# Performance work log

Measured on AMD Instinct MI355X. Metric: run time of the kernel, lower is better.

The kernel has to match this reference:

```python
import jax, jax.numpy as jnp
import numpy as np

B, T, D, H = 2, 2048, 2048, 16
d_head = D // H  # 128


def _rope(x):
    # x: [B, T, H, d]
    d = x.shape[-1]
    inv_freq = 1.0 / (10000.0 ** (jnp.arange(0, d, 2, dtype=jnp.float32) / d))
    t = jnp.arange(x.shape[1], dtype=jnp.float32)
    freqs = t[:, None] * inv_freq[None, :]          # [T, d/2]
    emb = jnp.concatenate([freqs, freqs], axis=-1)  # [T, d]
    cos = jnp.cos(emb)[None, :, None, :]
    sin = jnp.sin(emb)[None, :, None, :]
    x1, x2 = x[..., ::2], x[..., 1::2]
    rot = jnp.stack([-x2, x1], axis=-1).reshape(x.shape)
    return x * cos + rot * sin


def setup_inputs() -> dict:
    key = jax.random.key(0)
    ks = jax.random.split(key, 8)
    s = 1.0 / np.sqrt(D)
    return {
        "x": jax.random.normal(ks[0], (B, T, D), dtype=jnp.float32),
        "W_q": jax.random.normal(ks[1], (D, D), dtype=jnp.float32) * s,
        "W_k": jax.random.normal(ks[2], (D, D), dtype=jnp.float32) * s,
        "W_v": jax.random.normal(ks[3], (D, D), dtype=jnp.float32) * s,
        "W_gate": jax.random.normal(ks[4], (D, D), dtype=jnp.float32) * s,
        "W_p": jax.random.normal(ks[5], (D, D), dtype=jnp.float32) * s,
        "W_clock": jax.random.normal(ks[6], (D, H), dtype=jnp.float32) * s,
        "W_c": jax.random.normal(ks[7], (D, D), dtype=jnp.float32) * s,
    }


def _caps_forward(x, W_q, W_k, W_v, W_gate, W_p, W_clock, W_c):
    Bx, Tx, Dx = x.shape
    q = (x @ W_q).reshape(Bx, Tx, H, d_head)
    k = (x @ W_k).reshape(Bx, Tx, H, d_head)
    v = (x @ W_v).reshape(Bx, Tx, H, d_head)

    clock = jax.nn.softplus(x @ W_clock).reshape(Bx, Tx, H, 1) + 1e-6
    log_clock = jnp.log(clock)

    q = _rope(q)
    k = _rope(k)

    # Branch 1: p_exp normalization
    p = (x @ W_p).reshape(Bx, Tx, H, d_head) + log_clock
    p_max = jnp.max(p, axis=1, keepdims=True)
    p_exp = jnp.exp(p - p_max)
    p_cs = jnp.cumsum(p_exp, axis=1)
    q1 = q / (p_cs + 1e-8)
    k1 = k * p_exp

    # Branch 2: SPD gate cumprod via clipped cumsum
    gj = -jax.nn.softplus(x @ W_gate).reshape(Bx, Tx, H, d_head) * clock
    gj_cp = jnp.exp(jnp.clip(jnp.cumsum(gj, axis=1), -50.0, 40.0))
    q2 = q * gj_cp
    k2 = k / (gj_cp + 1e-8)

    # Branch 3: clock time scaling
    clock_cs = jnp.cumsum(clock, axis=1)
    q3 = q / clock_cs
    k3 = k * clock

    q_cat = jnp.concatenate([q1, q2, q3], axis=-1)  # [B,T,H,3d]
    k_cat = jnp.concatenate([k1, k2, k3], axis=-1)

    scale = 1.0 / jnp.sqrt(jnp.float32(3 * d_head))  # SDPA default: 1/sqrt(q last dim)
    scores = jnp.einsum('bthd,bshd->bhts', q_cat, k_cat) * scale
    attn = jax.nn.softmax(scores, axis=-1)
    out = jnp.einsum('bhts,bshd->bthd', attn, v).reshape(Bx, Tx, Dx)
    return out @ W_c


def reference(x, W_q, W_k, W_v, W_gate, W_p, W_clock, W_c):
    return _caps_forward(x, W_q, W_k, W_v, W_gate, W_p, W_clock, W_c)
```

## Files before the change

kernel.cpp:

```cpp
#include <hip/hip_runtime.h>

typedef unsigned short ushort;
typedef __attribute__((ext_vector_type(8))) short short8;
typedef __attribute__((ext_vector_type(4))) short short4v;
typedef __attribute__((ext_vector_type(4))) float f32x4;

#define Bb 2
#define Tt 2048
#define Dd 2048
#define Hh 16
#define Mm 4096
#define MD 8388608u

__device__ __forceinline__ float b2f(ushort u) {
  union { unsigned int ui; float f; } v; v.ui = ((unsigned int)u) << 16; return v.f;
}
__device__ __forceinline__ ushort f2b(float f) {
  union { float f; unsigned int u; } v; v.f = f;
  unsigned int r = (v.u + 0x7fffu + ((v.u >> 16) & 1u)) >> 16;
  return (ushort)r;
}
__device__ __forceinline__ void split3(float v, ushort& s0, ushort& s1, ushort& s2) {
  ushort a = f2b(v);        float f0 = b2f(a);
  float r1 = v - f0;        ushort b = f2b(r1);  float f1 = b2f(b);
  float r2 = r1 - f1;       ushort c = f2b(r2);
  s0 = a; s1 = b; s2 = c;
}
__device__ __forceinline__ void split3_rtz(float v, ushort& s0, ushort& s1, ushort& s2) {
  union { float f; unsigned u; } c; c.f = v;
  s0 = (ushort)(c.u >> 16);
  union { unsigned u; float f; } h; h.u = c.u & 0xffff0000u;
  float r1 = v - h.f;
  union { float f; unsigned u; } c1; c1.f = r1;
  s1 = (ushort)(c1.u >> 16);
  union { unsigned u; float f; } h1; h1.u = c1.u & 0xffff0000u;
  float r2 = r1 - h1.f;
  s2 = f2b(r2);
}
__device__ __forceinline__ void split2(float v, ushort& s0, ushort& s1) {
  union { float f; unsigned u; } c; c.f = v;
  s0 = (ushort)(c.u >> 16);
  union { unsigned u; float f; } h; h.u = c.u & 0xffff0000u;
  s1 = f2b(v - h.f);
}
__device__ __forceinline__ float softplusf(float x) {
  return fmaxf(x, 0.f) + log1pf(expf(-fabsf(x)));
}
__device__ __forceinline__ short4v tr16(unsigned a) {
  short4v d;
  asm volatile("ds_read_b64_tr_b16 %0, %1" : "=v"(d) : "v"(a));
  return d;
}

__global__ __launch_bounds__(256) void xsplit_k(const float* __restrict__ x,
                                                ushort* __restrict__ S0,
                                                ushort* __restrict__ S1,
                                                ushort* __restrict__ S2) {
  size_t i = ((size_t)blockIdx.x * 256 + threadIdx.x) * 8;
  float v[8];
  *(float4*)&v[0] = *(const float4*)(x + i);
  *(float4*)&v[4] = *(const float4*)(x + i + 4);
  ushort h0[8], h1[8], h2[8];
#pragma unroll
  for (int j = 0; j < 8; ++j) split3_rtz(v[j], h0[j], h1[j], h2[j]);
  *(uint4*)(S0 + i) = *(uint4*)h0;
  *(uint4*)(S1 + i) = *(uint4*)h1;
  *(uint4*)(S2 + i) = *(uint4*)h2;
}

template <int NP>
__global__ __launch_bounds__(256) void split_transposeN(const float* __restrict__ W,
                                                        ushort* __restrict__ T0,
                                                        ushort* __restrict__ T1,
                                                        ushort* __restrict__ T2) {
  __shared__ float tile[64][68];
  int k0 = blockIdx.x << 6, n0 = blockIdx.y << 6;
  int r = threadIdx.x >> 2, c0 = (threadIdx.x & 3) << 4;
  const float* src = W + (size_t)(k0 + r) * Dd + n0 + c0;
#pragma unroll
  for (int q = 0; q < 4; ++q)
    *(float4*)&tile[r][c0 + 4 * q] = *(const float4*)(src + 4 * q);
  __syncthreads();
  ushort h0[16], h1[16], h2[16];
#pragma unroll
  for (int i = 0; i < 16; ++i) {
    float v = tile[c0 + i][r];
    if (NP == 1) {
      h0[i] = f2b(v);
    } else if (NP == 2) {
      ushort a = f2b(v); h0[i] = a; h1[i] = f2b(v - b2f(a));
    } else {
      split3(v, h0[i], h1[i], h2[i]);
    }
  }
  size_t o = (size_t)(n0 + r) * Dd + k0 + c0;
  *(uint4*)(T0 + o) = *(uint4*)&h0[0];  *(uint4*)(T0 + o + 8) = *(uint4*)&h0[8];
  if (NP >= 2) { *(uint4*)(T1 + o) = *(uint4*)&h1[0];  *(uint4*)(T1 + o + 8) = *(uint4*)&h1[8]; }
  if (NP >= 3) { *(uint4*)(T2 + o) = *(uint4*)&h2[0];  *(uint4*)(T2 + o + 8) = *(uint4*)&h2[8]; }
}

__global__ __launch_bounds__(512) void gemm128_pre2(const ushort* __restrict__ A0,
                                                    const ushort* __restrict__ A1,
                                                    const ushort* __restrict__ B0,
                                                    const ushort* __restrict__ B1,
                                                    float* __restrict__ C) {
  const int N = 2048, K = 2048;
  int m0 = blockIdx.y << 7, n0 = blockIdx.x << 7;
  __shared__ ushort As0[8192], As1[8192], Bs0[8192], Bs1[8192];
  int tid = threadIdx.x;
  int row = tid >> 2, c0 = (tid & 3) << 4;
  int sw = row & 7, g0 = c0 >> 3;
  int dst0 = row * 64 + ((g0 ^ sw) << 3);
  int dst1 = row * 64 + (((g0 + 1) ^ sw) << 3);
  const ushort* a0p = A0 + (size_t)(m0 + row) * K + c0;
  const ushort* a1p = A1 + (size_t)(m0 + row) * K + c0;
  const ushort* b0p = B0 + (size_t)(n0 + row) * K + c0;
  const ushort* b1p = B1 + (size_t)(n0 + row) * K + c0;
  int lane = tid & 63, wave = tid >> 6;
  int l16 = lane & 15, quad = lane >> 4;
  int wm = (wave & 1) << 6, wn = (wave >> 1) << 5;
  f32x4 acc[4][2] = {};
  for (int k0 = 0; k0 < K; k0 += 64) {
    uint4 a00 = *(const uint4*)(a0p + k0), a01 = *(const uint4*)(a0p + k0 + 8);
    uint4 a10 = *(const uint4*)(a1p + k0), a11 = *(const uint4*)(a1p + k0 + 8);
    uint4 b00 = *(const uint4*)(b0p + k0), b01 = *(const uint4*)(b0p + k0 + 8);
    uint4 b10 = *(const uint4*)(b1p + k0), b11 = *(const uint4*)(b1p + k0 + 8);
    *(uint4*)&As0[dst0] = a00;  *(uint4*)&As0[dst1] = a01;
    *(uint4*)&As1[dst0] = a10;  *(uint4*)&As1[dst1] = a11;
    *(uint4*)&Bs0[dst0] = b00;  *(uint4*)&Bs0[dst1] = b01;
    *(uint4*)&Bs1[dst0] = b10;  *(uint4*)&Bs1[dst1] = b11;
    __syncthreads();
#pragma unroll
    for (int kk = 0; kk < 2; ++kk) {
      short8 af0[4], af1[4], bf0[2], bf1[2];
#pragma unroll
      for (int mi = 0; mi < 4; ++mi) {
        int rr = wm + (mi << 4) + l16;
        int g = (kk << 2) + quad;
        int idx = rr * 64 + ((g ^ (rr & 7)) << 3);
        af0[mi] = *(const short8*)&As0[idx];
        af1[mi] = *(const short8*)&As1[idx];
      }
#pragma unroll
      for (int nj = 0; nj < 2; ++nj) {
        int rr = wn + (nj << 4) + l16;
        int g = (kk << 2) + quad;
        int idx = rr * 64 + ((g ^ (rr & 7)) << 3);
        bf0[nj] = *(const short8*)&Bs0[idx];
        bf1[nj] = *(const short8*)&Bs1[idx];
      }
#pragma unroll
      for (int mi = 0; mi < 4; ++mi)
#pragma unroll
        for (int nj = 0; nj < 2; ++nj) {
          acc[mi][nj] = __builtin_amdgcn_mfma_f32_16x16x32_bf16(af1[mi], bf0[nj], acc[mi][nj], 0, 0, 0);
          acc[mi][nj] = __builtin_amdgcn_mfma_f32_16x16x32_bf16(af0[mi], bf1[nj], acc[mi][nj], 0, 0, 0);
          acc[mi][nj] = __builtin_amdgcn_mfma_f32_16x16x32_bf16(af0[mi], bf0[nj], acc[mi][nj], 0, 0, 0);
        }
    }
    __syncthreads();
  }
#pragma unroll
  for (int mi = 0; mi < 4; ++mi)
#pragma unroll
    for (int nj = 0; nj < 2; ++nj)
#pragma unroll
      for (int r = 0; r < 4; ++r) {
        int mm = m0 + wm + (mi << 4) + (quad << 2) + r;
        int nn = n0 + wn + (nj << 4) + l16;
        C[(size_t)mm * N + nn] = acc[mi][nj][r];
      }
}

template <int BF16OUT>
__global__ __launch_bounds__(512) void gemm128_split2(const float* __restrict__ A,
                                                      const ushort* __restrict__ B0,
                                                      const ushort* __restrict__ B1,
                                                      void* __restrict__ CBase) {
  const int N = 2048, K = 2048;
  int m0 = blockIdx.y << 7, n0 = blockIdx.x << 7;
  __shared__ ushort As0[8192], As1[8192], Bs0[8192], Bs1[8192];
  int tid = threadIdx.x;
  int row = tid >> 2, c0 = (tid & 3) << 4;
  int sw = row & 7, g0 = c0 >> 3;
  int dst0 = row * 64 + ((g0 ^ sw) << 3);
  int dst1 = row * 64 + (((g0 + 1) ^ sw) << 3);
  const float* aptr = A + (size_t)(m0 + row) * K + c0;
  const ushort* b0p = B0 + (size_t)(n0 + row) * K + c0;
  const ushort* b1p = B1 + (size_t)(n0 + row) * K + c0;
  int lane = tid & 63, wave = tid >> 6;
  int l16 = lane & 15, quad = lane >> 4;
  int wm = (wave & 1) << 6, wn = (wave >> 1) << 5;
  f32x4 acc[4][2] = {};
  for (int k0 = 0; k0 < K; k0 += 64) {
    float av[16];
#pragma unroll
    for (int q = 0; q < 4; ++q)
      *(float4*)&av[4 * q] = *(const float4*)(aptr + k0 + 4 * q);
    ushort a0[16], a1[16];
#pragma unroll
    for (int i = 0; i < 16; ++i) split2(av[i], a0[i], a1[i]);
    uint4 b00 = *(const uint4*)(b0p + k0), b01 = *(const uint4*)(b0p + k0 + 8);
    uint4 b10 = *(const uint4*)(b1p + k0), b11 = *(const uint4*)(b1p + k0 + 8);
    *(uint4*)&As0[dst0] = *(uint4*)&a0[0];  *(uint4*)&As0[dst1] = *(uint4*)&a0[8];
    *(uint4*)&As1[dst0] = *(uint4*)&a1[0];  *(uint4*)&As1[dst1] = *(uint4*)&a1[8];
    *(uint4*)&Bs0[dst0] = b00;  *(uint4*)&Bs0[dst1] = b01;
    *(uint4*)&Bs1[dst0] = b10;  *(uint4*)&Bs1[dst1] = b11;
    __syncthreads();
#pragma unroll
    for (int kk = 0; kk < 2; ++kk) {
      short8 af0[4], af1[4], bf0[2], bf1[2];
#pragma unroll
      for (int mi = 0; mi < 4; ++mi) {
        int rr = wm + (mi << 4) + l16;
        int g = (kk << 2) + quad;
        int idx = rr * 64 + ((g ^ (rr & 7)) << 3);
        af0[mi] = *(const short8*)&As0[idx];
        af1[mi] = *(const short8*)&As1[idx];
      }
#pragma unroll
      for (int nj = 0; nj < 2; ++nj) {
        int rr = wn + (nj << 4) + l16;
        int g = (kk << 2) + quad;
        int idx = rr * 64 + ((g ^ (rr & 7)) << 3);
        bf0[nj] = *(const short8*)&Bs0[idx];
        bf1[nj] = *(const short8*)&Bs1[idx];
      }
#pragma unroll
      for (int mi = 0; mi < 4; ++mi)
#pragma unroll
        for (int nj = 0; nj < 2; ++nj) {
          acc[mi][nj] = __builtin_amdgcn_mfma_f32_16x16x32_bf16(af1[mi], bf0[nj], acc[mi][nj], 0, 0, 0);
          acc[mi][nj] = __builtin_amdgcn_mfma_f32_16x16x32_bf16(af0[mi], bf1[nj], acc[mi][nj], 0, 0, 0);
          acc[mi][nj] = __builtin_amdgcn_mfma_f32_16x16x32_bf16(af0[mi], bf0[nj], acc[mi][nj], 0, 0, 0);
        }
    }
    __syncthreads();
  }
#pragma unroll
  for (int mi = 0; mi < 4; ++mi)
#pragma unroll
    for (int nj = 0; nj < 2; ++nj)
#pragma unroll
      for (int r = 0; r < 4; ++r) {
        int mm = m0 + wm + (mi << 4) + (quad << 2) + r;
        int nn = n0 + wn + (nj << 4) + l16;
        float v = acc[mi][nj][r];
        if (BF16OUT)
          ((ushort*)CBase)[(size_t)mm * N + nn] = f2b(v);
        else
          ((float*)CBase)[(size_t)mm * N + nn] = v;
      }
}

__global__ __launch_bounds__(512) void gemm128_b16(const ushort* __restrict__ A,
                                                   const ushort* __restrict__ Bt,
                                                   float* __restrict__ C) {
  const int N = 2048, K = 2048;
  int m0 = blockIdx.y << 7, n0 = blockIdx.x << 7;
  __shared__ ushort As[8192], Bs[8192];
  int tid = threadIdx.x;
  int row = tid >> 2, c0 = (tid & 3) << 4;
  int sw = row & 7, g0 = c0 >> 3;
  int dst0 = row * 64 + ((g0 ^ sw) << 3);
  int dst1 = row * 64 + (((g0 + 1) ^ sw) << 3);
  const ushort* aptr = A + (size_t)(m0 + row) * K + c0;
  const ushort* bptr = Bt + (size_t)(n0 + row) * K + c0;
  int lane = tid & 63, wave = tid >> 6;
  int l16 = lane & 15, quad = lane >> 4;
  int wm = (wave & 1) << 6, wn = (wave >> 1) << 5;
  f32x4 acc[4][2] = {};
  for (int k0 = 0; k0 < K; k0 += 64) {
    uint4 av0 = *(const uint4*)(aptr + k0), av1 = *(const uint4*)(aptr + k0 + 8);
    uint4 bv0 = *(const uint4*)(bptr + k0), bv1 = *(const uint4*)(bptr + k0 + 8);
    *(uint4*)&As[dst0] = av0;  *(uint4*)&As[dst1] = av1;
    *(uint4*)&Bs[dst0] = bv0;  *(uint4*)&Bs[dst1] = bv1;
    __syncthreads();
#pragma unroll
    for (int kk = 0; kk < 2; ++kk) {
      short8 af[4], bf[2];
#pragma unroll
      for (int mi = 0; mi < 4; ++mi) {
        int rr = wm + (mi << 4) + l16;
        int g = (kk << 2) + quad;
        af[mi] = *(const short8*)&As[rr * 64 + ((g ^ (rr & 7)) << 3)];
      }
#pragma unroll
      for (int nj = 0; nj < 2; ++nj) {
        int rr = wn + (nj << 4) + l16;
        int g = (kk << 2) + quad;
        bf[nj] = *(const short8*)&Bs[rr * 64 + ((g ^ (rr & 7)) << 3)];
      }
#pragma unroll
      for (int mi = 0; mi < 4; ++mi)
#pragma unroll
        for (int nj = 0; nj < 2; ++nj)
          acc[mi][nj] = __builtin_amdgcn_mfma_f32_16x16x32_bf16(af[mi], bf[nj], acc[mi][nj], 0, 0, 0);
    }
    __syncthreads();
  }
#pragma unroll
  for (int mi = 0; mi < 4; ++mi)
#pragma unroll
    for (int nj = 0; nj < 2; ++nj)
#pragma unroll
      for (int r = 0; r < 4; ++r) {
        int mm = m0 + wm + (mi << 4) + (quad << 2) + r;
        int nn = n0 + wn + (nj << 4) + l16;
        C[(size_t)mm * N + nn] = acc[mi][nj][r];
      }
}

__global__ __launch_bounds__(256) void gemm_pre(const ushort* __restrict__ A0,
                                                const ushort* __restrict__ A1,
                                                const ushort* __restrict__ A2,
                                                const ushort* __restrict__ B0,
                                                const ushort* __restrict__ B1,
                                                const ushort* __restrict__ B2,
                                                float* __restrict__ C) {
  const int N = 2048, K = 2048;
  int m0 = blockIdx.y << 6, n0 = blockIdx.x << 6;
  __shared__ ushort As0[4096], As1[4096], As2[4096];
  __shared__ ushort Bs0[4096], Bs1[4096], Bs2[4096];
  int tid = threadIdx.x;
  int row = tid >> 2, c0 = (tid & 3) << 4;
  int sw = row & 7;
  int g0 = c0 >> 3;
  int dst0 = row * 64 + ((g0 ^ sw) << 3);
  int dst1 = row * 64 + (((g0 + 1) ^ sw) << 3);
  const ushort* a0p = A0 + (size_t)(m0 + row) * K + c0;
  const ushort* a1p = A1 + (size_t)(m0 + row) * K + c0;
  const ushort* a2p = A2 + (size_t)(m0 + row) * K + c0;
  const ushort* b0p = B0 + (size_t)(n0 + row) * K + c0;
  const ushort* b1p = B1 + (size_t)(n0 + row) * K + c0;
  const ushort* b2p = B2 + (size_t)(n0 + row) * K + c0;
  int lane = tid & 63, wave = tid >> 6;
  int l16 = lane & 15, quad = lane >> 4;
  int wm = (wave & 1) << 5, wn = (wave >> 1) << 5;
  f32x4 acc[2][2] = {};
  for (int k0 = 0; k0 < K; k0 += 64) {
    uint4 a00 = *(const uint4*)(a0p + k0), a01 = *(const uint4*)(a0p + k0 + 8);
    uint4 a10 = *(const uint4*)(a1p + k0), a11 = *(const uint4*)(a1p + k0 + 8);
    uint4 a20 = *(const uint4*)(a2p + k0), a21 = *(const uint4*)(a2p + k0 + 8);
    uint4 b00 = *(const uint4*)(b0p + k0), b01 = *(const uint4*)(b0p + k0 + 8);
    uint4 b10 = *(const uint4*)(b1p + k0), b11 = *(const uint4*)(b1p + k0 + 8);
    uint4 b20 = *(const uint4*)(b2p + k0), b21 = *(const uint4*)(b2p + k0 + 8);
    *(uint4*)&As0[dst0] = a00;  *(uint4*)&As0[dst1] = a01;
    *(uint4*)&As1[dst0] = a10;  *(uint4*)&As1[dst1] = a11;
    *(uint4*)&As2[dst0] = a20;  *(uint4*)&As2[dst1] = a21;
    *(uint4*)&Bs0[dst0] = b00;  *(uint4*)&Bs0[dst1] = b01;
    *(uint4*)&Bs1[dst0] = b10;  *(uint4*)&Bs1[dst1] = b11;
    *(uint4*)&Bs2[dst0] = b20;  *(uint4*)&Bs2[dst1] = b21;
    __syncthreads();
#pragma unroll
    for (int kk = 0; kk < 2; ++kk) {
      short8 af0[2], af1[2], af2[2], bf0[2], bf1[2], bf2[2];
#pragma unroll
      for (int mi = 0; mi < 2; ++mi) {
        int rr = wm + (mi << 4) + l16;
        int g = (kk << 2) + quad;
        int idx = rr * 64 + ((g ^ (rr & 7)) << 3);
        af0[mi] = *(const short8*)&As0[idx];
        af1[mi] = *(const short8*)&As1[idx];
        af2[mi] = *(const short8*)&As2[idx];
      }
#pragma unroll
      for (int nj = 0; nj < 2; ++nj) {
        int rr = wn + (nj << 4) + l16;
        int g = (kk << 2) + quad;
        int idx = rr * 64 + ((g ^ (rr & 7)) << 3);
        bf0[nj] = *(const short8*)&Bs0[idx];
        bf1[nj] = *(const short8*)&Bs1[idx];
        bf2[nj] = *(const short8*)&Bs2[idx];
      }
#pragma unroll
      for (int mi = 0; mi < 2; ++mi)
#pragma unroll
        for (int nj = 0; nj < 2; ++nj) {
          acc[mi][nj] = __builtin_amdgcn_mfma_f32_16x16x32_bf16(af2[mi], bf0[nj], acc[mi][nj], 0, 0, 0);
          acc[mi][nj] = __builtin_amdgcn_mfma_f32_16x16x32_bf16(af0[mi], bf2[nj], acc[mi][nj], 0, 0, 0);
          acc[mi][nj] = __builtin_amdgcn_mfma_f32_16x16x32_bf16(af1[mi], bf1[nj], acc[mi][nj], 0, 0, 0);
          acc[mi][nj] = __builtin_amdgcn_mfma_f32_16x16x32_bf16(af1[mi], bf0[nj], acc[mi][nj], 0, 0, 0);
          acc[mi][nj] = __builtin_amdgcn_mfma_f32_16x16x32_bf16(af0[mi], bf1[nj], acc[mi][nj], 0, 0, 0);
          acc[mi][nj] = __builtin_amdgcn_mfma_f32_16x16x32_bf16(af0[mi], bf0[nj], acc[mi][nj], 0, 0, 0);
        }
    }
    __syncthreads();
  }
#pragma unroll
  for (int mi = 0; mi < 2; ++mi)
#pragma unroll
    for (int nj = 0; nj < 2; ++nj)
#pragma unroll
      for (int r = 0; r < 4; ++r) {
        int mm = m0 + wm + (mi << 4) + (quad << 2) + r;
        int nn = n0 + wn + (nj << 4) + l16;
        C[(size_t)mm * N + nn] = acc[mi][nj][r];
      }
}

__global__ __launch_bounds__(64) void wclock_k(const float* __restrict__ x,
                                               const float* __restrict__ Wc,
                                               float* __restrict__ out) {
  int m = blockIdx.x, lane = threadIdx.x;
  const float* xr = x + (size_t)m * Dd;
  float acc[16];
#pragma unroll
  for (int h = 0; h < 16; ++h) acc[h] = 0.f;
  for (int k = lane; k < Dd; k += 64) {
    float xv = xr[k];
    const float* wr = Wc + k * 16;
#pragma unroll
    for (int h = 0; h < 16; ++h) acc[h] += xv * wr[h];
  }
#pragma unroll
  for (int h = 0; h < 16; ++h) {
#pragma unroll
    for (int off = 32; off; off >>= 1) acc[h] += __shfl_down(acc[h], off);
  }
  if (lane == 0) {
    float* o = out + (size_t)m * 16;
#pragma unroll
    for (int h = 0; h < 16; ++h) o[h] = acc[h];
  }
}

__global__ __launch_bounds__(128) void pmaxchunk_k(const float* __restrict__ Pf,
                                                   const float* __restrict__ cpre,
                                                   float* __restrict__ pmaxc) {
  int bh = blockIdx.x, ch = blockIdx.y, d = threadIdx.x;
  int b = bh >> 4, h = bh & 15;
  float mx = -1e30f;
  int t0 = ch << 8;
  for (int t = t0; t < t0 + 256; ++t) {
    float pr = Pf[((size_t)(b * Tt + t)) * Dd + h * 128 + d];
    float c = softplusf(cpre[(b * Tt + t) * Hh + h]) + 1e-6f;
    mx = fmaxf(mx, pr + logf(c));
  }
  pmaxc[(size_t)(bh * 8 + ch) * 128 + d] = mx;
}

__global__ __launch_bounds__(128) void scan_ew_k(float* planes,
                                                 const float* __restrict__ cpre,
                                                 const float* __restrict__ pmaxc,
                                                 float* __restrict__ clockv,
                                                 float* __restrict__ sum_pe,
                                                 float* __restrict__ sum_gj,
                                                 float* __restrict__ sum_ck) {
  int ch = blockIdx.x, bh = blockIdx.y;
  int b = bh >> 4, h = bh & 15, d = threadIdx.x;
  float* Qf = planes;
  float* Kf = planes + (size_t)MD;
  float* Gf = planes + 2 * (size_t)MD;
  float* Pf = planes + 3 * (size_t)MD;
  float invf = (float)exp(-((double)((d & 63) * 2) / 128.0) * log(10000.0));
  float pmax = -1e30f;
#pragma unroll
  for (int c = 0; c < 8; ++c) pmax = fmaxf(pmax, pmaxc[(size_t)(bh * 8 + c) * 128 + d]);
  float s_pe = 0.f, s_gj = 0.f, s_ck = 0.f;
  int t0 = ch << 5;
#pragma unroll 4
  for (int i = 0; i < 32; ++i) {
    int t = t0 + i;
    size_t off = ((size_t)(b * Tt + t)) * Dd + h * 128 + d;
    float qv = Qf[off], kv = Kf[off], pv = Pf[off], gv = Gf[off];
    float clock = softplusf(cpre[(b * Tt + t) * Hh + h]) + 1e-6f;
    float ang = (float)t * invf;
    float c_ = cosf(ang), s_ = sinf(ang);
    float qp = __shfl_xor(qv, 1);
    float kp = __shfl_xor(kv, 1);
    float qrot = (d & 1) ? qp : -qp;
    float krot = (d & 1) ? kp : -kp;
    float qr = qv * c_ + qrot * s_;
    float kr = kv * c_ + krot * s_;
    float pe = expf(pv + logf(clock) - pmax);
    s_pe += pe;
    float gj = -softplusf(gv) * clock;
    s_gj += gj;
    Qf[off] = qr;
    Kf[off] = kr;
    Gf[off] = gj;
    Pf[off] = pe;
    if (d == 0) {
      clockv[bh * Tt + t] = clock;
      s_ck += clock;
    }
  }
  size_t so = (size_t)(bh * 64 + ch) * 128 + d;
  sum_pe[so] = s_pe;
  sum_gj[so] = s_gj;
  if (d == 0) sum_ck[bh * 64 + ch] = s_ck;
}

__global__ __launch_bounds__(128) void scan_off_k(const float* __restrict__ sum_pe,
                                                  const float* __restrict__ sum_gj,
                                                  const float* __restrict__ sum_ck,
                                                  float* __restrict__ pcs_cp,
                                                  float* __restrict__ goff,
                                                  float* __restrict__ coff) {
  int bh = blockIdx.x, d = threadIdx.x;
  float ppe = 0.f, pgj = 0.f, pck = 0.f;
  for (int c = 0; c < 64; ++c) {
    size_t o = (size_t)(bh * 64 + c) * 128 + d;
    pcs_cp[o] = ppe;
    goff[o] = pgj;
    ppe += sum_pe[o];
    pgj += sum_gj[o];
    if (d == 0) { coff[bh * 64 + c] = pck; pck += sum_ck[bh * 64 + c]; }
  }
}

__global__ __launch_bounds__(128) void scan_apply_k(float* planes,
                                                    const float* __restrict__ goff,
                                                    const float* __restrict__ coff,
                                                    const float* __restrict__ clockv,
                                                    float* __restrict__ ccsv) {
  int ch = blockIdx.x, bh = blockIdx.y;
  int b = bh >> 4, h = bh & 15, d = threadIdx.x;
  float* Gf = planes + 2 * (size_t)MD;
  float g = goff[(size_t)(bh * 64 + ch) * 128 + d];
  float ccs = (d == 0) ? coff[bh * 64 + ch] : 0.f;
  int t0 = ch << 5;
#pragma unroll 4
  for (int i = 0; i < 32; ++i) {
    int t = t0 + i;
    size_t off = ((size_t)(b * Tt + t)) * Dd + h * 128 + d;
    float gj = Gf[off];
    g += gj;
    float e = expf(fminf(fmaxf(g, -50.f), 40.f));
    Gf[off] = e;
    if (d == 0) {
      ccs += clockv[bh * Tt + t];
      ccsv[bh * Tt + t] = ccs;
    }
  }
}

__global__ __launch_bounds__(512, 2) void attn_mfma_k(const float* __restrict__ planes,
                                                      const ushort* __restrict__ Vb,
                                                      const float* __restrict__ clockv,
                                                      const float* __restrict__ ccsv,
                                                      const float* __restrict__ pcs_cp,
                                                      ushort* __restrict__ attnout) {
  __shared__ float smemf[18432];
  ushort* Khi = (ushort*)smemf;
  ushort* Klo = Khi + 12288;
  ushort* Vsm = Khi + 24576;
  unsigned* Pu = (unsigned*)(smemf + 14336);
  float* pcsL = smemf;
  ushort* qscr = (ushort*)(smemf + 8192);

  int tid = threadIdx.x;
  int lane = tid & 63, wave = tid >> 6;
  int l15 = lane & 15, qd = lane >> 4;
  int qt0 = blockIdx.x << 7;
  int bh = blockIdx.y, b = bh >> 4, h = bh & 15;
  const float* Qf = planes;
  const float* Kf = planes + (size_t)MD;
  const float* Ef = planes + 2 * (size_t)MD;
  const float* Pe = planes + 3 * (size_t)MD;
  size_t pbase = ((size_t)b * Tt) * Dd + h * 128;

  short8 qh[12], ql[12];
  int wl = wave & 3;
  int rloc = lane >> 2;
  {
    ushort* sh = qscr + (wl << 12);
    ushort* sl = sh + 2048;
#pragma unroll
    for (int rd = 0; rd < 2; ++rd) {
      if (tid < 256) {
        int d = tid & 127, seg = tid >> 7;
        int rbase = (rd << 6) + (seg << 5);
        float pcs = pcs_cp[((size_t)bh * 64 + (qt0 >> 5) + (rd << 1) + seg) * 128 + d];
        for (int i = 0; i < 32; ++i) {
          pcs += Pe[pbase + (size_t)(qt0 + rbase + i) * Dd + d];
          pcsL[((seg << 5) + i) * 128 + d] = pcs;
        }
      }
      __syncthreads();
      int part = ((wave >> 2) == rd);
      int grow = qt0 + (rd << 6) + (wl << 4) + rloc;
      float ccsr = __builtin_amdgcn_rcpf(ccsv[bh * Tt + grow]);
      size_t goffq = pbase + (size_t)grow * Dd;
#pragma unroll
      for (int cd = 0; cd < 3; ++cd) {
        __syncthreads();
        if (part) {
#pragma unroll
          for (int j = 0; j < 4; ++j) {
            int d0 = ((lane & 3) << 5) + (j << 3);
            float qv[8], mv[8];
            *(float4*)&qv[0] = *(const float4*)(Qf + goffq + d0);
            *(float4*)&qv[4] = *(const float4*)(Qf + goffq + d0 + 4);
            if (cd == 0) {
              *(float4*)&mv[0] = *(const float4*)&pcsL[((wl << 4) + rloc) * 128 + d0];
              *(float4*)&mv[4] = *(const float4*)&pcsL[((wl << 4) + rloc) * 128 + d0 + 4];
#pragma unroll
              for (int i = 0; i < 8; ++i) qv[i] = qv[i] * __builtin_amdgcn_rcpf(mv[i] + 1e-8f);
            } else if (cd == 1) {
              *(float4*)&mv[0] = *(const float4*)(Ef + goffq + d0);
              *(float4*)&mv[4] = *(const float4*)(Ef + goffq + d0 + 4);
#pragma unroll
              for (int i = 0; i < 8; ++i) qv[i] = qv[i] * mv[i];
            } else {
#pragma unroll
              for (int i = 0; i < 8; ++i) qv[i] = qv[i] * ccsr;
            }
            ushort hi8[8], lo8[8];
#pragma unroll
            for (int i = 0; i < 8; ++i) {
              ushort a = f2b(qv[i]); hi8[i] = a; lo8[i] = f2b(qv[i] - b2f(a));
            }
            int g = ((lane & 3) << 2) + j;
            int phys = (g & 8) | ((g ^ rloc) & 7);
            *(uint4*)&sh[rloc * 128 + (phys << 3)] = *(uint4*)hi8;
            *(uint4*)&sl[rloc * 128 + (phys << 3)] = *(uint4*)lo8;
          }
        }
        __syncthreads();
        if (part) {
#pragma unroll
          for (int ksl = 0; ksl < 4; ++ksl) {
            int g = (ksl << 2) + qd;
            int phys = (g & 8) | ((g ^ l15) & 7);
            qh[(cd << 2) + ksl] = *(const short8*)&sh[l15 * 128 + (phys << 3)];
            ql[(cd << 2) + ksl] = *(const short8*)&sl[l15 * 128 + (phys << 3)];
          }
        }
      }
      __syncthreads();
    }
  }

  float mi4[4], li4[4];
  f32x4 acc_pv[8] = {};
#pragma unroll
  for (int r = 0; r < 4; ++r) { mi4[r] = -1e30f; li4[r] = 0.f; }
  const float scl = 0.05103103630798287f;
  const ushort* vbase = Vb + pbase;
  unsigned* PuW = Pu + (wave << 9);
  unsigned VsmA = (unsigned)(size_t)Vsm;
  int kk = tid >> 4;
  int kdb = tid & 15;

  for (int st = 0; st < 64; ++st) {
    int s0 = st << 5;
    __syncthreads();
    {
      size_t roff = pbase + (size_t)(s0 + kk) * Dd + (kdb << 3);
      float ck = clockv[bh * Tt + s0 + kk];
      float kv[8], pev[8], ev[8];
      *(float4*)&kv[0] = *(const float4*)(Kf + roff);
      *(float4*)&kv[4] = *(const float4*)(Kf + roff + 4);
      *(float4*)&pev[0] = *(const float4*)(Pe + roff);
      *(float4*)&pev[4] = *(const float4*)(Pe + roff + 4);
      *(float4*)&ev[0] = *(const float4*)(Ef + roff);
      *(float4*)&ev[4] = *(const float4*)(Ef + roff + 4);
#pragma unroll
      for (int slot = 0; slot < 3; ++slot) {
        float val[8];
        if (slot == 0) {
#pragma unroll
          for (int i = 0; i < 8; ++i) val[i] = kv[i] * pev[i];
        } else if (slot == 1) {
#pragma unroll
          for (int i = 0; i < 8; ++i) val[i] = kv[i] * __builtin_amdgcn_rcpf(ev[i] + 1e-8f);
        } else {
#pragma unroll
          for (int i = 0; i < 8; ++i) val[i] = kv[i] * ck;
        }
        unsigned ub[8], ul[8];
#pragma unroll
        for (int i = 0; i < 8; ++i) {
          union { float f; unsigned u; } c; c.f = val[i];
          ub[i] = c.u;
          union { unsigned u; float f; } hm; hm.u = c.u & 0xffff0000u;
          union { float f; unsigned u; } lr; lr.f = val[i] - hm.f;
          ul[i] = lr.u;
        }
        uint4 hi4, lo4;
        hi4.x = (ub[0] >> 16) | (ub[1] & 0xffff0000u);
        hi4.y = (ub[2] >> 16) | (ub[3] & 0xffff0000u);
        hi4.z = (ub[4] >> 16) | (ub[5] & 0xffff0000u);
        hi4.w = (ub[6] >> 16) | (ub[7] & 0xffff0000u);
        lo4.x = (ul[0] >> 16) | (ul[1] & 0xffff0000u);
        lo4.y = (ul[2] >> 16) | (ul[3] & 0xffff0000u);
        lo4.z = (ul[4] >> 16) | (ul[5] & 0xffff0000u);
        lo4.w = (ul[6] >> 16) | (ul[7] & 0xffff0000u);
        int g = (slot << 4) + kdb;
        int phys = (g & ~7) | ((g ^ kk) & 7);
        *(uint4*)&Khi[kk * 384 + (phys << 3)] = hi4;
        *(uint4*)&Klo[kk * 384 + (phys << 3)] = lo4;
      }
      const ushort* vsrc = vbase + (size_t)(s0 + kk) * Dd + (kdb << 3);
      int vbyte = ((kdb >> 1) << 10) + (((kk >> 2) & 1) << 9) + ((kk >> 3) << 7) +
                  ((kk & 3) << 5) + ((kdb & 1) << 4);
      *(uint4*)((char*)Vsm + vbyte) = *(const uint4*)vsrc;
    }
    __syncthreads();
    f32x4 acc0 = {}, acc1 = {};
#pragma unroll
    for (int ks = 0; ks < 12; ++ks) {
      int g = (ks << 2) + qd;
      int p0i = (g & ~7) | ((g ^ l15) & 7);
      int p1i = (g & ~7) | ((g ^ (16 + l15)) & 7);
      short8 b0h = *(const short8*)&Khi[l15 * 384 + (p0i << 3)];
      short8 b0l = *(const short8*)&Klo[l15 * 384 + (p0i << 3)];
      short8 b1h = *(const short8*)&Khi[(16 + l15) * 384 + (p1i << 3)];
      short8 b1l = *(const short8*)&Klo[(16 + l15) * 384 + (p1i << 3)];
      acc0 = __builtin_amdgcn_mfma_f32_16x16x32_bf16(ql[ks], b0h, acc0, 0, 0, 0);
      acc0 = __builtin_amdgcn_mfma_f32_16x16x32_bf16(qh[ks], b0l, acc0, 0, 0, 0);
      acc0 = __builtin_amdgcn_mfma_f32_16x16x32_bf16(qh[ks], b0h, acc0, 0, 0, 0);
      acc1 = __builtin_amdgcn_mfma_f32_16x16x32_bf16(ql[ks], b1h, acc1, 0, 0, 0);
      acc1 = __builtin_amdgcn_mfma_f32_16x16x32_bf16(qh[ks], b1l, acc1, 0, 0, 0);
      acc1 = __builtin_amdgcn_mfma_f32_16x16x32_bf16(qh[ks], b1h, acc1, 0, 0, 0);
    }
#pragma unroll
    for (int r = 0; r < 4; ++r) {
      float sa = acc0[r] * scl, sb = acc1[r] * scl;
      float mx = fmaxf(sa, sb);
#pragma unroll
      for (int m = 1; m < 16; m <<= 1) mx = fmaxf(mx, __shfl_xor(mx, m));
      float mn = fmaxf(mi4[r], mx);
      float al = expf(mi4[r] - mn);
      float p0 = expf(sa - mn), p1 = expf(sb - mn);
      float rs = p0 + p1;
#pragma unroll
      for (int m = 1; m < 16; m <<= 1) rs += __shfl_xor(rs, m);
      li4[r] = li4[r] * al + rs;
      mi4[r] = mn;
#pragma unroll
      for (int n0 = 0; n0 < 8; ++n0) acc_pv[n0][r] *= al;
      int R = (qd << 2) + r;
      {
        union { float f; unsigned u; } c0, c1; c0.f = p0; c1.f = p1;
        union { unsigned u; float f; } m0_, m1_;
        m0_.u = c0.u & 0xffff0000u; m1_.u = c1.u & 0xffff0000u;
        union { float f; unsigned u; } d0_, d1_;
        d0_.f = p0 - m0_.f; d1_.f = p1 - m1_.f;
        unsigned u0 = (c0.u >> 16) | (d0_.u & 0xffff0000u);
        unsigned u1 = (c1.u >> 16) | (d1_.u & 0xffff0000u);
        int r7 = R & 7;
        char* pb = (char*)PuW + (R << 7) + ((l15 & 3) << 2);
        *(unsigned*)(pb + (((l15 >> 2) ^ r7) << 4)) = u0;
        *(unsigned*)(pb + ((((l15 >> 2) + 4) ^ r7) << 4)) = u1;
      }
    }
    {
      unsigned pw[8];
      {
        const char* pb = (const char*)PuW + l15 * 128;
        uint4 w0 = *(const uint4*)(pb + ((((qd << 1)) ^ (l15 & 7)) << 4));
        uint4 w1 = *(const uint4*)(pb + ((((qd << 1) | 1) ^ (l15 & 7)) << 4));
        pw[0] = w0.x; pw[1] = w0.y; pw[2] = w0.z; pw[3] = w0.w;
        pw[4] = w1.x; pw[5] = w1.y; pw[6] = w1.z; pw[7] = w1.w;
      }
      union { unsigned u[4]; short8 s; } uph, upl;
#pragma unroll
      for (int i = 0; i < 4; ++i) {
        uph.u[i] = (pw[2 * i] & 0xffffu) | (pw[2 * i + 1] << 16);
        upl.u[i] = (pw[2 * i] >> 16) | (pw[2 * i + 1] & 0xffff0000u);
      }
      short4v tv[16];
#pragma unroll
      for (int n0 = 0; n0 < 8; ++n0) {
        unsigned a0 = VsmA + (n0 << 10) + (lane << 3);
        tv[2 * n0] = tr16(a0);
        tv[2 * n0 + 1] = tr16(a0 + 512);
      }
      asm volatile("s_waitcnt lgkmcnt(0)" ::: "memory");
      __builtin_amdgcn_sched_barrier(0);
#pragma unroll
      for (int n0 = 0; n0 < 8; ++n0) {
        short8 bv = __builtin_shufflevector(tv[2 * n0], tv[2 * n0 + 1], 0, 1, 2, 3, 4, 5, 6, 7);
        acc_pv[n0] = __builtin_amdgcn_mfma_f32_16x16x32_bf16(uph.s, bv, acc_pv[n0], 0, 0, 0);
        acc_pv[n0] = __builtin_amdgcn_mfma_f32_16x16x32_bf16(upl.s, bv, acc_pv[n0], 0, 0, 0);
      }
    }
  }
#pragma unroll
  for (int r = 0; r < 4; ++r) {
    float inv = 1.f / li4[r];
    int trow = qt0 + (wave << 4) + (qd << 2) + r;
    ushort* orow = attnout + ((size_t)(b * Tt + trow)) * Dd + h * 128 + l15;
#pragma unroll
    for (int n0 = 0; n0 < 8; ++n0)
      orow[n0 << 4] = f2b(acc_pv[n0][r] * inv);
  }
}

extern "C" void kernel_launch(void* const* d_in, const int* in_sizes, int n_in,
                              void* d_out, int out_size, void* d_ws, size_t ws_size,
                              hipStream_t stream) {
  const float* x = (const float*)d_in[0];
  const float* Wq = (const float*)d_in[1];
  const float* Wk = (const float*)d_in[2];
  const float* Wv = (const float*)d_in[3];
  const float* Wg = (const float*)d_in[4];
  const float* Wp = (const float*)d_in[5];
  const float* Wclk = (const float*)d_in[6];
  const float* Wc = (const float*)d_in[7];

  float* planes = (float*)d_ws;
  float* Aq = planes;
  float* Bk = planes + (size_t)MD;
  float* Ce = planes + 2 * (size_t)MD;
  float* Dp = planes + 3 * (size_t)MD;
  ushort* Vb = (ushort*)(planes + 4 * (size_t)MD);
  float* cpre = (float*)(Vb + (size_t)MD);
  float* clockv = cpre + 65536;
  float* ccsv = clockv + 65536;
  float* pmaxc = ccsv + 65536;
  float* pcs_cp = pmaxc + 32768;
  ushort* Wt0 = (ushort*)(pcs_cp + 262144);
  ushort* Wt1 = Wt0 + (size_t)Dd * Dd;
  ushort* Wt2 = Wt1 + (size_t)Dd * Dd;
  ushort* attnout = Wt0;
  ushort* WcT0 = (ushort*)Ce;
  ushort* xs0 = (ushort*)Dp;
  ushort* xs1 = xs0 + (size_t)MD;
  ushort* xs2 = (ushort*)Vb;
  float* sum_pe = (float*)Wt2;
  float* sum_gj = sum_pe + 262144;
  float* goff_  = sum_gj + 262144;
  float* sum_ck = goff_ + 262144;
  float* coff_  = sum_ck + 2048;

  size_t needed = (size_t)((char*)(Wt2 + (size_t)Dd * Dd) - (char*)d_ws);
  if (ws_size < needed) return;

  dim3 tg(Dd / 64, Dd / 64);
  dim3 g128(Dd / 128, Mm / 128), gg(Dd / 64, Mm / 64);

  xsplit_k<<<dim3(MD / 8 / 256), 256, 0, stream>>>(x, xs0, xs1, xs2);

  split_transposeN<2><<<tg, 256, 0, stream>>>(Wq, Wt0, Wt1, nullptr);
  gemm128_pre2<<<g128, 512, 0, stream>>>(xs0, xs1, Wt0, Wt1, Aq);
  split_transposeN<2><<<tg, 256, 0, stream>>>(Wk, Wt0, Wt1, nullptr);
  gemm128_pre2<<<g128, 512, 0, stream>>>(xs0, xs1, Wt0, Wt1, Bk);
  split_transposeN<3><<<tg, 256, 0, stream>>>(Wg, Wt0, Wt1, Wt2);
  gemm_pre<<<gg, 256, 0, stream>>>(xs0, xs1, xs2, Wt0, Wt1, Wt2, Ce);
  split_transposeN<2><<<tg, 256, 0, stream>>>(Wp, Wt0, Wt1, nullptr);
  gemm128_split2<0><<<g128, 512, 0, stream>>>(x, Wt0, Wt1, (void*)Dp);
  split_transposeN<2><<<tg, 256, 0, stream>>>(Wv, Wt0, Wt1, nullptr);
  gemm128_split2<1><<<g128, 512, 0, stream>>>(x, Wt0, Wt1, (void*)Vb);

  wclock_k<<<dim3(Mm), dim3(64), 0, stream>>>(x, Wclk, cpre);
  pmaxchunk_k<<<dim3(Bb * Hh, 8), dim3(128), 0, stream>>>(Dp, cpre, pmaxc);

  scan_ew_k<<<dim3(64, Bb * Hh), dim3(128), 0, stream>>>(planes, cpre, pmaxc, clockv,
                                                         sum_pe, sum_gj, sum_ck);
  scan_off_k<<<dim3(Bb * Hh), dim3(128), 0, stream>>>(sum_pe, sum_gj, sum_ck,
                                                      pcs_cp, goff_, coff_);
  scan_apply_k<<<dim3(64, Bb * Hh), dim3(128), 0, stream>>>(planes, goff_, coff_, clockv, ccsv);

  attn_mfma_k<<<dim3(Tt / 128, Bb * Hh), dim3(512), 0, stream>>>(planes, Vb, clockv, ccsv, pcs_cp, attnout);

  split_transposeN<1><<<tg, 256, 0, stream>>>(Wc, WcT0, nullptr, nullptr);
  gemm128_b16<<<g128, 512, 0, stream>>>(attnout, WcT0, (float*)d_out);
}
```

Before: 1.712 ms.

## Drop three-way split for gate GEMM, widen pmax reduction, raise MFMA priority

The gate projection drops its 3-plane bf16 split (6 MFMAs per tile in a 64x64 GEMM) for the 2-plane 128x128 gemm128_pre2 path. The x split now produces only two planes, and the third weight plane goes away. pmaxchunk_k now uses 512 threads, each covering a quarter of the time chunk, and combines the partial maxima through shared memory. s_setprio is raised around the MFMA loops in attention. Gate precision drops, which matters because gj feeds an exp of a cumulative sum.

```diff
diff --git a/kernel.cpp b/kernel.cpp
--- a/kernel.cpp
+++ b/kernel.cpp
@@ -20,23 +20,6 @@
   unsigned int r = (v.u + 0x7fffu + ((v.u >> 16) & 1u)) >> 16;
   return (ushort)r;
 }
-__device__ __forceinline__ void split3(float v, ushort& s0, ushort& s1, ushort& s2) {
-  ushort a = f2b(v);        float f0 = b2f(a);
-  float r1 = v - f0;        ushort b = f2b(r1);  float f1 = b2f(b);
-  float r2 = r1 - f1;       ushort c = f2b(r2);
-  s0 = a; s1 = b; s2 = c;
-}
-__device__ __forceinline__ void split3_rtz(float v, ushort& s0, ushort& s1, ushort& s2) {
-  union { float f; unsigned u; } c; c.f = v;
-  s0 = (ushort)(c.u >> 16);
-  union { unsigned u; float f; } h; h.u = c.u & 0xffff0000u;
-  float r1 = v - h.f;
-  union { float f; unsigned u; } c1; c1.f = r1;
-  s1 = (ushort)(c1.u >> 16);
-  union { unsigned u; float f; } h1; h1.u = c1.u & 0xffff0000u;
-  float r2 = r1 - h1.f;
-  s2 = f2b(r2);
-}
 __device__ __forceinline__ void split2(float v, ushort& s0, ushort& s1) {
   union { float f; unsigned u; } c; c.f = v;
   s0 = (ushort)(c.u >> 16);
@@ -52,27 +35,24 @@
   return d;
 }
 
-__global__ __launch_bounds__(256) void xsplit_k(const float* __restrict__ x,
-                                                ushort* __restrict__ S0,
-                                                ushort* __restrict__ S1,
-                                                ushort* __restrict__ S2) {
+__global__ __launch_bounds__(256) void xsplit2_k(const float* __restrict__ x,
+                                                 ushort* __restrict__ S0,
+                                                 ushort* __restrict__ S1) {
   size_t i = ((size_t)blockIdx.x * 256 + threadIdx.x) * 8;
   float v[8];
   *(float4*)&v[0] = *(const float4*)(x + i);
   *(float4*)&v[4] = *(const float4*)(x + i + 4);
-  ushort h0[8], h1[8], h2[8];
-#pragma unroll
-  for (int j = 0; j < 8; ++j) split3_rtz(v[j], h0[j], h1[j], h2[j]);
+  ushort h0[8], h1[8];
+#pragma unroll
+  for (int j = 0; j < 8; ++j) split2(v[j], h0[j], h1[j]);
   *(uint4*)(S0 + i) = *(uint4*)h0;
   *(uint4*)(S1 + i) = *(uint4*)h1;
-  *(uint4*)(S2 + i) = *(uint4*)h2;
 }
 
 template <int NP>
 __global__ __launch_bounds__(256) void split_transposeN(const float* __restrict__ W,
                                                         ushort* __restrict__ T0,
-                                                        ushort* __restrict__ T1,
-                                                        ushort* __restrict__ T2) {
+                                                        ushort* __restrict__ T1) {
   __shared__ float tile[64][68];
   int k0 = blockIdx.x << 6, n0 = blockIdx.y << 6;
   int r = threadIdx.x >> 2, c0 = (threadIdx.x & 3) << 4;
@@ -81,22 +61,19 @@
   for (int q = 0; q < 4; ++q)
     *(float4*)&tile[r][c0 + 4 * q] = *(const float4*)(src + 4 * q);
   __syncthreads();
-  ushort h0[16], h1[16], h2[16];
+  ushort h0[16], h1[16];
 #pragma unroll
   for (int i = 0; i < 16; ++i) {
     float v = tile[c0 + i][r];
     if (NP == 1) {
       h0[i] = f2b(v);
-    } else if (NP == 2) {
+    } else {
       ushort a = f2b(v); h0[i] = a; h1[i] = f2b(v - b2f(a));
-    } else {
-      split3(v, h0[i], h1[i], h2[i]);
     }
   }
   size_t o = (size_t)(n0 + r) * Dd + k0 + c0;
   *(uint4*)(T0 + o) = *(uint4*)&h0[0];  *(uint4*)(T0 + o + 8) = *(uint4*)&h0[8];
   if (NP >= 2) { *(uint4*)(T1 + o) = *(uint4*)&h1[0];  *(uint4*)(T1 + o + 8) = *(uint4*)&h1[8]; }
-  if (NP >= 3) { *(uint4*)(T2 + o) = *(uint4*)&h2[0];  *(uint4*)(T2 + o + 8) = *(uint4*)&h2[8]; }
 }
 
 __global__ __launch_bounds__(512) void gemm128_pre2(const ushort* __restrict__ A0,
@@ -311,94 +288,6 @@
       }
 }
 
-__global__ __launch_bounds__(256) void gemm_pre(const ushort* __restrict__ A0,
-                                                const ushort* __restrict__ A1,
-                                                const ushort* __restrict__ A2,
-                                                const ushort* __restrict__ B0,
-                                                const ushort* __restrict__ B1,
-                                                const ushort* __restrict__ B2,
-                                                float* __restrict__ C) {
-  const int N = 2048, K = 2048;
-  int m0 = blockIdx.y << 6, n0 = blockIdx.x << 6;
-  __shared__ ushort As0[4096], As1[4096], As2[4096];
-  __shared__ ushort Bs0[4096], Bs1[4096], Bs2[4096];
-  int tid = threadIdx.x;
-  int row = tid >> 2, c0 = (tid & 3) << 4;
-  int sw = row & 7;
-  int g0 = c0 >> 3;
-  int dst0 = row * 64 + ((g0 ^ sw) << 3);
-  int dst1 = row * 64 + (((g0 + 1) ^ sw) << 3);
-  const ushort* a0p = A0 + (size_t)(m0 + row) * K + c0;
-  const ushort* a1p = A1 + (size_t)(m0 + row) * K + c0;
-  const ushort* a2p = A2 + (size_t)(m0 + row) * K + c0;
-  const ushort* b0p = B0 + (size_t)(n0 + row) * K + c0;
-  const ushort* b1p = B1 + (size_t)(n0 + row) * K + c0;
-  const ushort* b2p = B2 + (size_t)(n0 + row) * K + c0;
-  int lane = tid & 63, wave = tid >> 6;
-  int l16 = lane & 15, quad = lane >> 4;
-  int wm = (wave & 1) << 5, wn = (wave >> 1) << 5;
-  f32x4 acc[2][2] = {};
-  for (int k0 = 0; k0 < K; k0 += 64) {
-    uint4 a00 = *(const uint4*)(a0p + k0), a01 = *(const uint4*)(a0p + k0 + 8);
-    uint4 a10 = *(const uint4*)(a1p + k0), a11 = *(const uint4*)(a1p + k0 + 8);
-    uint4 a20 = *(const uint4*)(a2p + k0), a21 = *(const uint4*)(a2p + k0 + 8);
-    uint4 b00 = *(const uint4*)(b0p + k0), b01 = *(const uint4*)(b0p + k0 + 8);
-    uint4 b10 = *(const uint4*)(b1p + k0), b11 = *(const uint4*)(b1p + k0 + 8);
-    uint4 b20 = *(const uint4*)(b2p + k0), b21 = *(const uint4*)(b2p + k0 + 8);
-    *(uint4*)&As0[dst0] = a00;  *(uint4*)&As0[dst1] = a01;
-    *(uint4*)&As1[dst0] = a10;  *(uint4*)&As1[dst1] = a11;
-    *(uint4*)&As2[dst0] = a20;  *(uint4*)&As2[dst1] = a21;
-    *(uint4*)&Bs0[dst0] = b00;  *(uint4*)&Bs0[dst1] = b01;
-    *(uint4*)&Bs1[dst0] = b10;  *(uint4*)&Bs1[dst1] = b11;
-    *(uint4*)&Bs2[dst0] = b20;  *(uint4*)&Bs2[dst1] = b21;
-    __syncthreads();
-#pragma unroll
-    for (int kk = 0; kk < 2; ++kk) {
-      short8 af0[2], af1[2], af2[2], bf0[2], bf1[2], bf2[2];
-#pragma unroll
-      for (int mi = 0; mi < 2; ++mi) {
-        int rr = wm + (mi << 4) + l16;
-        int g = (kk << 2) + quad;
-        int idx = rr * 64 + ((g ^ (rr & 7)) << 3);
-        af0[mi] = *(const short8*)&As0[idx];
-        af1[mi] = *(const short8*)&As1[idx];
-        af2[mi] = *(const short8*)&As2[idx];
-      }
-#pragma unroll
-      for (int nj = 0; nj < 2; ++nj) {
-        int rr = wn + (nj << 4) + l16;
-        int g = (kk << 2) + quad;
-        int idx = rr * 64 + ((g ^ (rr & 7)) << 3);
-        bf0[nj] = *(const short8*)&Bs0[idx];
-        bf1[nj] = *(const short8*)&Bs1[idx];
-        bf2[nj] = *(const short8*)&Bs2[idx];
-      }
-#pragma unroll
-      for (int mi = 0; mi < 2; ++mi)
-#pragma unroll
-        for (int nj = 0; nj < 2; ++nj) {
-          acc[mi][nj] = __builtin_amdgcn_mfma_f32_16x16x32_bf16(af2[mi], bf0[nj], acc[mi][nj], 0, 0, 0);
-          acc[mi][nj] = __builtin_amdgcn_mfma_f32_16x16x32_bf16(af0[mi], bf2[nj], acc[mi][nj], 0, 0, 0);
-          acc[mi][nj] = __builtin_amdgcn_mfma_f32_16x16x32_bf16(af1[mi], bf1[nj], acc[mi][nj], 0, 0, 0);
-          acc[mi][nj] = __builtin_amdgcn_mfma_f32_16x16x32_bf16(af1[mi], bf0[nj], acc[mi][nj], 0, 0, 0);
-          acc[mi][nj] = __builtin_amdgcn_mfma_f32_16x16x32_bf16(af0[mi], bf1[nj], acc[mi][nj], 0, 0, 0);
-          acc[mi][nj] = __builtin_amdgcn_mfma_f32_16x16x32_bf16(af0[mi], bf0[nj], acc[mi][nj], 0, 0, 0);
-        }
-    }
-    __syncthreads();
-  }
-#pragma unroll
-  for (int mi = 0; mi < 2; ++mi)
-#pragma unroll
-    for (int nj = 0; nj < 2; ++nj)
-#pragma unroll
-      for (int r = 0; r < 4; ++r) {
-        int mm = m0 + wm + (mi << 4) + (quad << 2) + r;
-        int nn = n0 + wn + (nj << 4) + l16;
-        C[(size_t)mm * N + nn] = acc[mi][nj][r];
-      }
-}
-
 __global__ __launch_bounds__(64) void wclock_k(const float* __restrict__ x,
                                                const float* __restrict__ Wc,
                                                float* __restrict__ out) {
@@ -425,19 +314,25 @@
   }
 }
 
-__global__ __launch_bounds__(128) void pmaxchunk_k(const float* __restrict__ Pf,
+__global__ __launch_bounds__(512) void pmaxchunk_k(const float* __restrict__ Pf,
                                                    const float* __restrict__ cpre,
                                                    float* __restrict__ pmaxc) {
-  int bh = blockIdx.x, ch = blockIdx.y, d = threadIdx.x;
+  __shared__ float red[4][128];
+  int bh = blockIdx.x, ch = blockIdx.y;
+  int d = threadIdx.x & 127, qtr = threadIdx.x >> 7;
   int b = bh >> 4, h = bh & 15;
   float mx = -1e30f;
-  int t0 = ch << 8;
-  for (int t = t0; t < t0 + 256; ++t) {
+  int t0 = (ch << 8) + (qtr << 6);
+  for (int t = t0; t < t0 + 64; ++t) {
     float pr = Pf[((size_t)(b * Tt + t)) * Dd + h * 128 + d];
     float c = softplusf(cpre[(b * Tt + t) * Hh + h]) + 1e-6f;
     mx = fmaxf(mx, pr + logf(c));
   }
-  pmaxc[(size_t)(bh * 8 + ch) * 128 + d] = mx;
+  red[qtr][d] = mx;
+  __syncthreads();
+  if (qtr == 0)
+    pmaxc[(size_t)(bh * 8 + ch) * 128 + d] =
+        fmaxf(fmaxf(red[0][d], red[1][d]), fmaxf(red[2][d], red[3][d]));
 }
 
 __global__ __launch_bounds__(128) void scan_ew_k(float* planes,
@@ -700,6 +595,7 @@
     }
     __syncthreads();
     f32x4 acc0 = {}, acc1 = {};
+    __builtin_amdgcn_s_setprio(1);
 #pragma unroll
     for (int ks = 0; ks < 12; ++ks) {
       int g = (ks << 2) + qd;
@@ -716,6 +612,7 @@
       acc1 = __builtin_amdgcn_mfma_f32_16x16x32_bf16(qh[ks], b1l, acc1, 0, 0, 0);
       acc1 = __builtin_amdgcn_mfma_f32_16x16x32_bf16(qh[ks], b1h, acc1, 0, 0, 0);
     }
+    __builtin_amdgcn_s_setprio(0);
 #pragma unroll
     for (int r = 0; r < 4; ++r) {
       float sa = acc0[r] * scl, sb = acc1[r] * scl;
@@ -771,12 +668,14 @@
       }
       asm volatile("s_waitcnt lgkmcnt(0)" ::: "memory");
       __builtin_amdgcn_sched_barrier(0);
+      __builtin_amdgcn_s_setprio(1);
 #pragma unroll
       for (int n0 = 0; n0 < 8; ++n0) {
         short8 bv = __builtin_shufflevector(tv[2 * n0], tv[2 * n0 + 1], 0, 1, 2, 3, 4, 5, 6, 7);
         acc_pv[n0] = __builtin_amdgcn_mfma_f32_16x16x32_bf16(uph.s, bv, acc_pv[n0], 0, 0, 0);
         acc_pv[n0] = __builtin_amdgcn_mfma_f32_16x16x32_bf16(upl.s, bv, acc_pv[n0], 0, 0, 0);
       }
+      __builtin_amdgcn_s_setprio(0);
     }
   }
 #pragma unroll
@@ -820,7 +719,6 @@
   ushort* WcT0 = (ushort*)Ce;
   ushort* xs0 = (ushort*)Dp;
   ushort* xs1 = xs0 + (size_t)MD;
-  ushort* xs2 = (ushort*)Vb;
   float* sum_pe = (float*)Wt2;
   float* sum_gj = sum_pe + 262144;
   float* goff_  = sum_gj + 262144;
@@ -831,23 +729,23 @@
   if (ws_size < needed) return;
 
   dim3 tg(Dd / 64, Dd / 64);
-  dim3 g128(Dd / 128, Mm / 128), gg(Dd / 64, Mm / 64);
-
-  xsplit_k<<<dim3(MD / 8 / 256), 256, 0, stream>>>(x, xs0, xs1, xs2);
-
-  split_transposeN<2><<<tg, 256, 0, stream>>>(Wq, Wt0, Wt1, nullptr);
+  dim3 g128(Dd / 128, Mm / 128);
+
+  xsplit2_k<<<dim3(MD / 8 / 256), 256, 0, stream>>>(x, xs0, xs1);
+
+  split_transposeN<2><<<tg, 256, 0, stream>>>(Wq, Wt0, Wt1);
   gemm128_pre2<<<g128, 512, 0, stream>>>(xs0, xs1, Wt0, Wt1, Aq);
-  split_transposeN<2><<<tg, 256, 0, stream>>>(Wk, Wt0, Wt1, nullptr);
+  split_transposeN<2><<<tg, 256, 0, stream>>>(Wk, Wt0, Wt1);
   gemm128_pre2<<<g128, 512, 0, stream>>>(xs0, xs1, Wt0, Wt1, Bk);
-  split_transposeN<3><<<tg, 256, 0, stream>>>(Wg, Wt0, Wt1, Wt2);
-  gemm_pre<<<gg, 256, 0, stream>>>(xs0, xs1, xs2, Wt0, Wt1, Wt2, Ce);
-  split_transposeN<2><<<tg, 256, 0, stream>>>(Wp, Wt0, Wt1, nullptr);
+  split_transposeN<2><<<tg, 256, 0, stream>>>(Wg, Wt0, Wt1);
+  gemm128_pre2<<<g128, 512, 0, stream>>>(xs0, xs1, Wt0, Wt1, Ce);
+  split_transposeN<2><<<tg, 256, 0, stream>>>(Wp, Wt0, Wt1);
   gemm128_split2<0><<<g128, 512, 0, stream>>>(x, Wt0, Wt1, (void*)Dp);
-  split_transposeN<2><<<tg, 256, 0, stream>>>(Wv, Wt0, Wt1, nullptr);
+  split_transposeN<2><<<tg, 256, 0, stream>>>(Wv, Wt0, Wt1);
   gemm128_split2<1><<<g128, 512, 0, stream>>>(x, Wt0, Wt1, (void*)Vb);
 
   wclock_k<<<dim3(Mm), dim3(64), 0, stream>>>(x, Wclk, cpre);
-  pmaxchunk_k<<<dim3(Bb * Hh, 8), dim3(128), 0, stream>>>(Dp, cpre, pmaxc);
+  pmaxchunk_k<<<dim3(Bb * Hh, 8), dim3(512), 0, stream>>>(Dp, cpre, pmaxc);
 
   scan_ew_k<<<dim3(64, Bb * Hh), dim3(128), 0, stream>>>(planes, cpre, pmaxc, clockv,
                                                          sum_pe, sum_gj, sum_ck);
@@ -857,6 +755,6 @@
 
   attn_mfma_k<<<dim3(Tt / 128, Bb * Hh), dim3(512), 0, stream>>>(planes, Vb, clockv, ccsv, pcs_cp, attnout);
 
-  split_transposeN<1><<<tg, 256, 0, stream>>>(Wc, WcT0, nullptr, nullptr);
+  split_transposeN<1><<<tg, 256, 0, stream>>>(Wc, WcT0, nullptr);
   gemm128_b16<<<g128, 512, 0, stream>>>(attnout, WcT0, (float*)d_out);
 }
```

Result: faster. 1.533 ms (-10.5%).
